# Kernel optimization log

Measured on AMD Instinct MI355X. Metric: run time of the kernel, lower is better.

Reference implementation:

```python
import jax, jax.numpy as jnp
import numpy as np

N, OBS, ENC, ACT, K = 16384, 512, 512, 64, 8
ALPHA = 1.0


def setup_inputs() -> dict:
    key = jax.random.key(0)
    ks = jax.random.split(key, 8)
    s = 0.05  # keep activations/logits well-scaled
    return {
        "X1": jax.random.normal(ks[0], (N, OBS), jnp.float32),
        "X0": jax.random.normal(ks[1], (N, OBS), jnp.float32),
        "U": jax.random.normal(ks[2], (N, ACT), jnp.float32),
        "W_enc": jax.random.normal(ks[3], (ENC, OBS), jnp.float32) * s,
        "A_all": jax.random.normal(ks[4], (K, ENC, ENC), jnp.float32) * s,
        "B_rest": jax.random.normal(ks[5], (K - 1, ACT, ENC), jnp.float32) * s,
        "C_w": jax.random.normal(ks[6], (K, ENC), jnp.float32) * s,
        "C_b": jax.random.normal(ks[7], (K,), jnp.float32) * s,
    }


def reference(X1, X0, U, W_enc, A_all, B_rest, C_w, C_b):
    enc_dim = W_enc.shape[0]
    act_dim = U.shape[1]
    k = A_all.shape[0]
    # encoder: bias-free linear
    X1e = X1 @ W_enc.T  # [N, enc]
    X0e = X0 @ W_enc.T  # [N, enc]
    # gating: argmax of linear classifier C
    inds = jnp.argmax(X0e @ C_w.T + C_b, axis=1)  # [N]
    # expert 0 uses fixed B0 = eye(enc)[:act, :]; experts 1..k-1 learned
    B0 = jnp.eye(enc_dim, dtype=X0.dtype)[:act_dim]  # [act, enc]
    B_all = jnp.concatenate([B0[None], B_rest], axis=0)  # [k, act, enc]
    # per-expert predictions for every row (nn.Linear: x @ W.T -> einsum over input dim h)
    preds = jnp.einsum('nh,keh->kne', X0e, A_all) + jnp.einsum('na,kae->kne', U, B_all)
    # squared error per (expert, row), then select each row's routed expert
    sq = jnp.sum((X1e[None, :, :] - preds) ** 2, axis=-1)  # [k, N]
    onehot = jax.nn.one_hot(inds, k, dtype=sq.dtype)  # [N, k]
    loss = ALPHA * jnp.sum(sq * onehot.T)
    return loss / (enc_dim * X1.shape[0])
```

## Files before the change

### kernel.cpp

```cpp
#include <hip/hip_runtime.h>

#define NROWS 16384
#define OBSD 512
#define ENCD 512
#define ACTD 64
#define KEXP 8

typedef __attribute__((ext_vector_type(8))) short bf16x8;
typedef __attribute__((ext_vector_type(4))) float f32x4;
typedef __attribute__((address_space(3))) unsigned char lds_byte;
typedef __attribute__((address_space(1))) unsigned char glb_byte;

__device__ __forceinline__ unsigned short f2bf(float f) {
  unsigned int u = __float_as_uint(f);
  u = (u + 0x7FFFu + ((u >> 16) & 1u)) >> 16;
  return (unsigned short)u;
}
__device__ __forceinline__ float bf2f(unsigned short h) {
  return __uint_as_float(((unsigned int)h) << 16);
}
__device__ __forceinline__ unsigned int cvtpk(float lo, float hi) {
  unsigned int r;
  asm("v_cvt_pk_bf16_f32 %0, %1, %2" : "=v"(r) : "v"(lo), "v"(hi));
  return r;
}
__device__ __forceinline__ void gload_lds16(const unsigned short* g, unsigned short* l) {
  __builtin_amdgcn_global_load_lds((const glb_byte*)g, (lds_byte*)l, 16, 0, 0);
}

__global__ __launch_bounds__(256) void prep2_k(
    const float* __restrict__ U, const float* __restrict__ W,
    const float* __restrict__ Aall, const float* __restrict__ Brest,
    const float* __restrict__ Cw,
    unsigned short* __restrict__ Ubf, unsigned short* __restrict__ Wbf,
    unsigned short* __restrict__ Abf, unsigned short* __restrict__ BfT,
    float* __restrict__ GT, float* __restrict__ loss,
    int* __restrict__ counts, int* __restrict__ cursor) {
  const int b = blockIdx.x, tid = threadIdx.x;
  if (b < 64) {
    __shared__ float red[4][64];
    int e = b >> 3, o0 = (b & 7) * 64;
    int o = tid & 63, hg = tid >> 6;
    float s = 0.f;
#pragma unroll 8
    for (int h = hg * 128; h < hg * 128 + 128; h++)
      s += Cw[e * ENCD + h] * W[(size_t)h * OBSD + o0 + o];
    red[hg][o] = s;
    __syncthreads();
    if (tid < 64)
      GT[(o0 + tid) * KEXP + e] = red[0][tid] + red[1][tid] + red[2][tid] + red[3][tid];
    return;
  }
  if (b == 64) {
    if (tid == 0) *loss = 0.f;
    if (tid < KEXP) { counts[tid] = 0; cursor[tid] = 0; }
    return;
  }
  if (b == 65) {
    for (int j = 0; j < 16; j++) {
      int i8 = j * 256 + tid;
      int e = i8 >> 3, a0 = (i8 & 7) * 8;
      unsigned int w0 = 0, w1 = 0, w2 = 0, w3 = 0;
      if (e >= a0 && e < a0 + 8) {
        unsigned int bits = 0x3F80u << ((e & 1) * 16);
        if ((e - a0) >> 1 == 0) w0 = bits;
        else if ((e - a0) >> 1 == 1) w1 = bits;
        else if ((e - a0) >> 1 == 2) w2 = bits;
        else w3 = bits;
      }
      uint4 v = {w0, w1, w2, w3};
      *(uint4*)&BfT[(size_t)i8 * 8] = v;
    }
    return;
  }
  if (b < 122) {
    __shared__ float tile[64][65];
    int t = b - 66;
    int k = (t >> 3);
    int e0 = (t & 7) * 64;
    const float* src = Brest + (size_t)k * ACTD * ENCD + e0;
#pragma unroll
    for (int j = 0; j < 16; j++) {
      int idx = j * 256 + tid;
      int a = idx >> 6, e = idx & 63;
      tile[a][e] = src[(size_t)a * ENCD + e];
    }
    __syncthreads();
    unsigned short* dst = BfT + ((size_t)(k + 1) * ENCD + e0) * ACTD;
#pragma unroll
    for (int j = 0; j < 16; j++) {
      int idx = j * 256 + tid;
      int e = idx >> 6, a = idx & 63;
      dst[(size_t)e * ACTD + a] = f2bf(tile[a][e]);
    }
    return;
  }
  int cb = b - 122;
  const float* src;
  unsigned short* dst;
  size_t i;
  if (cb < 1024)      { src = U;    dst = Ubf; i = (size_t)cb * 256 + tid; }
  else if (cb < 1280) { src = W;    dst = Wbf; i = (size_t)(cb - 1024) * 256 + tid; }
  else                { src = Aall; dst = Abf; i = (size_t)(cb - 1280) * 256 + tid; }
  float4 v = ((const float4*)src)[i];
  uint2 r = {cvtpk(v.x, v.y), cvtpk(v.z, v.w)};
  *(uint2*)&dst[i * 4] = r;
}

__global__ __launch_bounds__(256) void routing_cvt_k(
    const float* __restrict__ X0, const float* __restrict__ X1,
    const float* __restrict__ GT, const float* __restrict__ Cb,
    unsigned short* __restrict__ X0bf, unsigned short* __restrict__ X1bf,
    int* __restrict__ inds, int* __restrict__ counts) {
  const int b = blockIdx.x, tid = threadIdx.x;
  if (b >= 512) {
    size_t i = ((size_t)(b - 512) * 256 + tid) * 8;
    const float4* s4 = (const float4*)(X1 + i);
    float4 a = s4[0], c = s4[1];
    uint4 r = {cvtpk(a.x, a.y), cvtpk(a.z, a.w), cvtpk(c.x, c.y), cvtpk(c.z, c.w)};
    *(uint4*)&X1bf[i] = r;
    return;
  }
  __shared__ int lhist[KEXP];
  if (tid < KEXP) lhist[tid] = 0;
  __syncthreads();
  const int lane = tid & 63, w = tid >> 6;
  float g[8][8];
  const float* gp = GT + lane * 8 * KEXP;
#pragma unroll
  for (int j = 0; j < 8; j++) {
    float4 lo = *(const float4*)(gp + j * KEXP);
    float4 hi = *(const float4*)(gp + j * KEXP + 4);
    g[j][0] = lo.x; g[j][1] = lo.y; g[j][2] = lo.z; g[j][3] = lo.w;
    g[j][4] = hi.x; g[j][5] = hi.y; g[j][6] = hi.z; g[j][7] = hi.w;
  }
  float cb[KEXP];
#pragma unroll
  for (int e = 0; e < KEXP; e++) cb[e] = Cb[e];

#pragma unroll 2
  for (int r = 0; r < 8; r++) {
    const int n = b * 32 + w * 8 + r;
    const float4* xr = (const float4*)(X0 + (size_t)n * OBSD + lane * 8);
    float4 x = xr[0], y = xr[1];
    float xv[8] = {x.x, x.y, x.z, x.w, y.x, y.y, y.z, y.w};
    float acc[KEXP] = {};
#pragma unroll
    for (int j = 0; j < 8; j++)
#pragma unroll
      for (int e = 0; e < KEXP; e++) acc[e] += xv[j] * g[j][e];
    uint4 rr = {cvtpk(x.x, x.y), cvtpk(x.z, x.w), cvtpk(y.x, y.y), cvtpk(y.z, y.w)};
    *(uint4*)&X0bf[(size_t)n * OBSD + lane * 8] = rr;
#pragma unroll
    for (int e = 0; e < KEXP; e++) {
#pragma unroll
      for (int off = 32; off > 0; off >>= 1) acc[e] += __shfl_xor(acc[e], off, 64);
    }
    if (lane == 0) {
      int best = 0;
      float bv = acc[0] + cb[0];
#pragma unroll
      for (int e = 1; e < KEXP; e++) {
        float v = acc[e] + cb[e];
        if (v > bv) { bv = v; best = e; }
      }
      inds[n] = best;
      atomicAdd(&lhist[best], 1);
    }
  }
  __syncthreads();
  if (tid < KEXP) atomicAdd(&counts[tid], lhist[tid]);
}

__global__ void prefix_k(const int* __restrict__ counts, int* __restrict__ cursor,
                         int* __restrict__ starts) {
  if (threadIdx.x == 0 && blockIdx.x == 0) {
    int s = 0;
    for (int k = 0; k < KEXP; k++) { starts[k] = s; cursor[k] = s; s += counts[k]; }
    starts[KEXP] = s;
  }
}

__global__ __launch_bounds__(256) void scatter_k(
    const int* __restrict__ inds, int* __restrict__ cursor,
    int* __restrict__ rowlist) {
  __shared__ int lhist[KEXP], lbase[KEXP];
  const int tid = threadIdx.x;
  if (tid < KEXP) lhist[tid] = 0;
  __syncthreads();
  const int n = blockIdx.x * 256 + tid;
  const int r = inds[n];
  const int lpos = atomicAdd(&lhist[r], 1);
  __syncthreads();
  if (tid < KEXP) lbase[tid] = atomicAdd(&cursor[tid], lhist[tid]);
  __syncthreads();
  rowlist[lbase[r] + lpos] = n;
}

__global__ __launch_bounds__(256, 2) void enc_mfma_k(
    const unsigned short* __restrict__ X1bf, const unsigned short* __restrict__ X0bf,
    const unsigned short* __restrict__ Wbf, unsigned short* __restrict__ X1e,
    unsigned short* __restrict__ X0e) {
  __shared__ unsigned short As[128 * 32];
  __shared__ unsigned short Bs[128 * 32];
  const int tid = threadIdx.x;
  const int bid = blockIdx.x;
  const int lid = (bid & 7) * 128 + (bid >> 3);
  const int lz = lid >> 9;
  const int rem = lid & 511;
  const int col0 = (rem & 3) * 128;
  const int row0 = (rem >> 2) * 128;
  const unsigned short* X = lz ? X0bf : X1bf;
  unsigned short* E = lz ? X0e : X1e;

  const int lane = tid & 63, w = tid >> 6;
  const int wr = w >> 1, wc = w & 1;
  const int gslot = ((tid & 3) ^ ((tid >> 3) & 3)) * 8;
  const int srow = tid >> 2;
  const int ldsoff = tid * 8;
  const int rslot = ((lane >> 4) ^ (((lane & 15) >> 1) & 3)) * 8;
  const int arow = wr * 64 + (lane & 15);
  const int brow = wc * 64 + (lane & 15);

  f32x4 acc[4][4] = {};
  for (int k0 = 0; k0 < OBSD; k0 += 32) {
    gload_lds16(X + (size_t)(row0 + srow) * OBSD + k0 + gslot, &As[ldsoff]);
    gload_lds16(X + (size_t)(row0 + 64 + srow) * OBSD + k0 + gslot, &As[2048 + ldsoff]);
    gload_lds16(Wbf + (size_t)(col0 + srow) * OBSD + k0 + gslot, &Bs[ldsoff]);
    gload_lds16(Wbf + (size_t)(col0 + 64 + srow) * OBSD + k0 + gslot, &Bs[2048 + ldsoff]);
    __syncthreads();
    bf16x8 af[4], bfr[4];
#pragma unroll
    for (int m = 0; m < 4; m++) af[m] = *(const bf16x8*)&As[(arow + m * 16) * 32 + rslot];
#pragma unroll
    for (int n = 0; n < 4; n++) bfr[n] = *(const bf16x8*)&Bs[(brow + n * 16) * 32 + rslot];
#pragma unroll
    for (int m = 0; m < 4; m++)
#pragma unroll
      for (int n = 0; n < 4; n++)
        acc[m][n] = __builtin_amdgcn_mfma_f32_16x16x32_bf16(bfr[n], af[m], acc[m][n], 0, 0, 0);
    __syncthreads();
  }
#pragma unroll
  for (int m = 0; m < 4; m++) {
    int rowg = row0 + wr * 64 + m * 16 + (lane & 15);
#pragma unroll
    for (int n = 0; n < 4; n++) {
      int colg = col0 + wc * 64 + n * 16 + (lane >> 4) * 4;
      uint2 v = {cvtpk(acc[m][n][0], acc[m][n][1]), cvtpk(acc[m][n][2], acc[m][n][3])};
      *(uint2*)&E[(size_t)rowg * ENCD + colg] = v;
    }
  }
}

__global__ __launch_bounds__(256, 2) void grouped_mfma_k(
    const unsigned short* __restrict__ X0ebf, const unsigned short* __restrict__ X1ebf,
    const unsigned short* __restrict__ Ubf, const unsigned short* __restrict__ Abf,
    const unsigned short* __restrict__ BfTbf, const int* __restrict__ rowlist,
    const int* __restrict__ starts, float* __restrict__ loss) {
  const int tid = threadIdx.x;
  const int bid = blockIdx.x;
  const int lid = (bid & 7) * 512 + (bid >> 3);
  const int k = lid >> 9;
  const int rem = lid & 511;
  const int col0 = (rem & 3) * 128;
  const int tile = rem >> 2;

  const int start = starts[k];
  const int cnt = starts[k + 1] - start;
  if (tile * 128 >= cnt) return;

  __shared__ unsigned short As[128 * 32];
  __shared__ unsigned short Bs[128 * 32];
  __shared__ int ridx[128];
  __shared__ float red[4];

  if (tid < 128) {
    int p = tile * 128 + tid;
    ridx[tid] = rowlist[start + (p < cnt ? p : 0)];
  }
  __syncthreads();

  const int lane = tid & 63, w = tid >> 6;
  const int wr = w >> 1, wc = w & 1;
  const int gslot = ((tid & 3) ^ ((tid >> 3) & 3)) * 8;
  const int srow = tid >> 2;
  const int ldsoff = tid * 8;
  const int rslot = ((lane >> 4) ^ (((lane & 15) >> 1) & 3)) * 8;
  const int arow = wr * 64 + (lane & 15);
  const int brow = wc * 64 + (lane & 15);
  const int rn0 = ridx[srow];
  const int rn1 = ridx[64 + srow];

  f32x4 acc[4][4] = {};
  const unsigned short* Ak = Abf + (size_t)k * ENCD * ENCD;
  for (int k0 = 0; k0 < ENCD; k0 += 32) {
    gload_lds16(X0ebf + (size_t)rn0 * ENCD + k0 + gslot, &As[ldsoff]);
    gload_lds16(X0ebf + (size_t)rn1 * ENCD + k0 + gslot, &As[2048 + ldsoff]);
    gload_lds16(Ak + (size_t)(col0 + srow) * ENCD + k0 + gslot, &Bs[ldsoff]);
    gload_lds16(Ak + (size_t)(col0 + 64 + srow) * ENCD + k0 + gslot, &Bs[2048 + ldsoff]);
    __syncthreads();
    bf16x8 af[4], bfr[4];
#pragma unroll
    for (int m = 0; m < 4; m++) af[m] = *(const bf16x8*)&As[(arow + m * 16) * 32 + rslot];
#pragma unroll
    for (int n = 0; n < 4; n++) bfr[n] = *(const bf16x8*)&Bs[(brow + n * 16) * 32 + rslot];
#pragma unroll
    for (int m = 0; m < 4; m++)
#pragma unroll
      for (int n = 0; n < 4; n++)
        acc[m][n] = __builtin_amdgcn_mfma_f32_16x16x32_bf16(bfr[n], af[m], acc[m][n], 0, 0, 0);
    __syncthreads();
  }
  const unsigned short* BfTk = BfTbf + (size_t)k * ENCD * ACTD;
  for (int a0 = 0; a0 < ACTD; a0 += 32) {
    gload_lds16(Ubf + (size_t)rn0 * ACTD + a0 + gslot, &As[ldsoff]);
    gload_lds16(Ubf + (size_t)rn1 * ACTD + a0 + gslot, &As[2048 + ldsoff]);
    gload_lds16(BfTk + (size_t)(col0 + srow) * ACTD + a0 + gslot, &Bs[ldsoff]);
    gload_lds16(BfTk + (size_t)(col0 + 64 + srow) * ACTD + a0 + gslot, &Bs[2048 + ldsoff]);
    __syncthreads();
    bf16x8 af[4], bfr[4];
#pragma unroll
    for (int m = 0; m < 4; m++) af[m] = *(const bf16x8*)&As[(arow + m * 16) * 32 + rslot];
#pragma unroll
    for (int n = 0; n < 4; n++) bfr[n] = *(const bf16x8*)&Bs[(brow + n * 16) * 32 + rslot];
#pragma unroll
    for (int m = 0; m < 4; m++)
#pragma unroll
      for (int n = 0; n < 4; n++)
        acc[m][n] = __builtin_amdgcn_mfma_f32_16x16x32_bf16(bfr[n], af[m], acc[m][n], 0, 0, 0);
    __syncthreads();
  }
  float sq = 0.f;
#pragma unroll
  for (int m = 0; m < 4; m++) {
    int lr = wr * 64 + m * 16 + (lane & 15);
    bool valid = (tile * 128 + lr) < cnt;
    const unsigned short* xrow = X1ebf + (size_t)ridx[lr] * ENCD;
#pragma unroll
    for (int n = 0; n < 4; n++) {
      int cg = col0 + wc * 64 + n * 16 + (lane >> 4) * 4;
      if (valid) {
        ushort4 x4 = *(const ushort4*)&xrow[cg];
        float d0 = bf2f(x4.x) - acc[m][n][0];
        float d1 = bf2f(x4.y) - acc[m][n][1];
        float d2 = bf2f(x4.z) - acc[m][n][2];
        float d3 = bf2f(x4.w) - acc[m][n][3];
        sq += d0 * d0 + d1 * d1 + d2 * d2 + d3 * d3;
      }
    }
  }
#pragma unroll
  for (int off = 32; off > 0; off >>= 1) sq += __shfl_xor(sq, off, 64);
  if (lane == 0) red[w] = sq;
  __syncthreads();
  if (tid == 0) atomicAdd(loss, red[0] + red[1] + red[2] + red[3]);
}

__global__ void finalize_k(const float* __restrict__ loss, float* __restrict__ out) {
  if (threadIdx.x == 0 && blockIdx.x == 0)
    out[0] = loss[0] * (1.0f / ((float)ENCD * (float)NROWS));
}

extern "C" void kernel_launch(void* const* d_in, const int* in_sizes, int n_in,
                              void* d_out, int out_size, void* d_ws, size_t ws_size,
                              hipStream_t stream) {
  const float* X1 = (const float*)d_in[0];
  const float* X0 = (const float*)d_in[1];
  const float* U = (const float*)d_in[2];
  const float* W = (const float*)d_in[3];
  const float* Aall = (const float*)d_in[4];
  const float* Brest = (const float*)d_in[5];
  const float* Cw = (const float*)d_in[6];
  const float* Cb = (const float*)d_in[7];
  float* out = (float*)d_out;

  char* p = (char*)d_ws;
  auto alloc = [&](size_t bytes) { char* r = p; p += (bytes + 255) & ~(size_t)255; return r; };
  unsigned short* X1bf = (unsigned short*)alloc((size_t)NROWS * OBSD * 2);
  unsigned short* X0bf = (unsigned short*)alloc((size_t)NROWS * OBSD * 2);
  unsigned short* Ubf = (unsigned short*)alloc((size_t)NROWS * ACTD * 2);
  unsigned short* Wbf = (unsigned short*)alloc((size_t)ENCD * OBSD * 2);
  unsigned short* Abf = (unsigned short*)alloc((size_t)KEXP * ENCD * ENCD * 2);
  unsigned short* BfT = (unsigned short*)alloc((size_t)KEXP * ENCD * ACTD * 2);
  unsigned short* X1ebf = (unsigned short*)alloc((size_t)NROWS * ENCD * 2);
  unsigned short* X0ebf = (unsigned short*)alloc((size_t)NROWS * ENCD * 2);
  float* GT = (float*)alloc(KEXP * OBSD * 4);
  float* loss = (float*)alloc(256);
  int* inds = (int*)alloc(NROWS * 4);
  int* rowlist = (int*)alloc(NROWS * 4);
  int* counts = (int*)alloc(64);
  int* cursor = (int*)alloc(64);
  int* starts = (int*)alloc(64);

  prep2_k<<<3450, 256, 0, stream>>>(U, W, Aall, Brest, Cw, Ubf, Wbf, Abf, BfT,
                                    GT, loss, counts, cursor);
  routing_cvt_k<<<512 + 4096, 256, 0, stream>>>(X0, X1, GT, Cb, X0bf, X1bf,
                                                inds, counts);
  prefix_k<<<1, 1, 0, stream>>>(counts, cursor, starts);
  scatter_k<<<NROWS / 256, 256, 0, stream>>>(inds, cursor, rowlist);

  enc_mfma_k<<<1024, 256, 0, stream>>>(X1bf, X0bf, Wbf, X1ebf, X0ebf);
  grouped_mfma_k<<<4096, 256, 0, stream>>>(X0ebf, X1ebf, Ubf, Abf, BfT,
                                           rowlist, starts, loss);
  finalize_k<<<1, 64, 0, stream>>>(loss, out);
}
```

Before: 92.74 us.

## Regroup prep kernels, fuse scatter into encoder GEMM, deepen encoder K-tile

Splits out a small GT kernel and merges the weight, X1 and X0 routing conversions into one large fused prep launch. The row scatter now runs as extra blocks of the encoder GEMM kernel, removing a separate launch. The encoder GEMM K-step grows from 32 to 64 with a new 8-slot XOR swizzle, halving the barrier count per tile at the cost of doubled LDS. The net effect is fewer launches and fewer syncs, with a risk of lower occupancy from the larger shared buffers.

```diff
diff --git a/kernel.cpp b/kernel.cpp
--- a/kernel.cpp
+++ b/kernel.cpp
@@ -28,35 +28,120 @@
   __builtin_amdgcn_global_load_lds((const glb_byte*)g, (lds_byte*)l, 16, 0, 0);
 }
 
-__global__ __launch_bounds__(256) void prep2_k(
-    const float* __restrict__ U, const float* __restrict__ W,
-    const float* __restrict__ Aall, const float* __restrict__ Brest,
-    const float* __restrict__ Cw,
-    unsigned short* __restrict__ Ubf, unsigned short* __restrict__ Wbf,
-    unsigned short* __restrict__ Abf, unsigned short* __restrict__ BfT,
+__global__ __launch_bounds__(256) void gt_k(
+    const float* __restrict__ W, const float* __restrict__ Cw,
     float* __restrict__ GT, float* __restrict__ loss,
     int* __restrict__ counts, int* __restrict__ cursor) {
   const int b = blockIdx.x, tid = threadIdx.x;
-  if (b < 64) {
-    __shared__ float red[4][64];
-    int e = b >> 3, o0 = (b & 7) * 64;
-    int o = tid & 63, hg = tid >> 6;
-    float s = 0.f;
-#pragma unroll 8
-    for (int h = hg * 128; h < hg * 128 + 128; h++)
-      s += Cw[e * ENCD + h] * W[(size_t)h * OBSD + o0 + o];
-    red[hg][o] = s;
-    __syncthreads();
-    if (tid < 64)
-      GT[(o0 + tid) * KEXP + e] = red[0][tid] + red[1][tid] + red[2][tid] + red[3][tid];
-    return;
-  }
-  if (b == 64) {
+  if (b == 0) {
     if (tid == 0) *loss = 0.f;
     if (tid < KEXP) { counts[tid] = 0; cursor[tid] = 0; }
+  }
+  __shared__ float red[4][64];
+  int e = b >> 3, o0 = (b & 7) * 64;
+  int o = tid & 63, hg = tid >> 6;
+  float s = 0.f;
+#pragma unroll 8
+  for (int h = hg * 128; h < hg * 128 + 128; h++)
+    s += Cw[e * ENCD + h] * W[(size_t)h * OBSD + o0 + o];
+  red[hg][o] = s;
+  __syncthreads();
+  if (tid < 64)
+    GT[(o0 + tid) * KEXP + e] = red[0][tid] + red[1][tid] + red[2][tid] + red[3][tid];
+}
+
+__global__ __launch_bounds__(256) void fused_prep_k(
+    const float* __restrict__ X0, const float* __restrict__ X1,
+    const float* __restrict__ U, const float* __restrict__ W,
+    const float* __restrict__ Aall, const float* __restrict__ Brest,
+    const float* __restrict__ GT, const float* __restrict__ Cb,
+    unsigned short* __restrict__ X0bf, unsigned short* __restrict__ X1bf,
+    unsigned short* __restrict__ Ubf, unsigned short* __restrict__ Wbf,
+    unsigned short* __restrict__ Abf, unsigned short* __restrict__ BfT,
+    int* __restrict__ inds, int* __restrict__ counts) {
+  const int b = blockIdx.x, tid = threadIdx.x;
+  if (b < 512) {
+    __shared__ int lhist[KEXP];
+    if (tid < KEXP) lhist[tid] = 0;
+    __syncthreads();
+    const int lane = tid & 63, w = tid >> 6;
+    float g[8][8];
+    const float* gp = GT + lane * 8 * KEXP;
+#pragma unroll
+    for (int j = 0; j < 8; j++) {
+      float4 lo = *(const float4*)(gp + j * KEXP);
+      float4 hi = *(const float4*)(gp + j * KEXP + 4);
+      g[j][0] = lo.x; g[j][1] = lo.y; g[j][2] = lo.z; g[j][3] = lo.w;
+      g[j][4] = hi.x; g[j][5] = hi.y; g[j][6] = hi.z; g[j][7] = hi.w;
+    }
+    float cb[KEXP];
+#pragma unroll
+    for (int e = 0; e < KEXP; e++) cb[e] = Cb[e];
+#pragma unroll 2
+    for (int r = 0; r < 8; r++) {
+      const int n = b * 32 + w * 8 + r;
+      const float4* xr = (const float4*)(X0 + (size_t)n * OBSD + lane * 8);
+      float4 x = xr[0], y = xr[1];
+      float xv[8] = {x.x, x.y, x.z, x.w, y.x, y.y, y.z, y.w};
+      float acc[KEXP] = {};
+#pragma unroll
+      for (int j = 0; j < 8; j++)
+#pragma unroll
+        for (int e = 0; e < KEXP; e++) acc[e] += xv[j] * g[j][e];
+      uint4 rr = {cvtpk(x.x, x.y), cvtpk(x.z, x.w), cvtpk(y.x, y.y), cvtpk(y.z, y.w)};
+      *(uint4*)&X0bf[(size_t)n * OBSD + lane * 8] = rr;
+#pragma unroll
+      for (int e = 0; e < KEXP; e++) {
+#pragma unroll
+        for (int off = 32; off > 0; off >>= 1) acc[e] += __shfl_xor(acc[e], off, 64);
+      }
+      if (lane == 0) {
+        int best = 0;
+        float bv = acc[0] + cb[0];
+#pragma unroll
+        for (int e = 1; e < KEXP; e++) {
+          float v = acc[e] + cb[e];
+          if (v > bv) { bv = v; best = e; }
+        }
+        inds[n] = best;
+        atomicAdd(&lhist[best], 1);
+      }
+    }
+    __syncthreads();
+    if (tid < KEXP) atomicAdd(&counts[tid], lhist[tid]);
     return;
   }
-  if (b == 65) {
+  if (b < 4608) {
+    size_t i = ((size_t)(b - 512) * 256 + tid) * 8;
+    const float4* s4 = (const float4*)(X1 + i);
+    float4 a = s4[0], c = s4[1];
+    uint4 r = {cvtpk(a.x, a.y), cvtpk(a.z, a.w), cvtpk(c.x, c.y), cvtpk(c.z, c.w)};
+    *(uint4*)&X1bf[i] = r;
+    return;
+  }
+  if (b < 4664) {
+    __shared__ float tile[64][65];
+    int t = b - 4608;
+    int k = (t >> 3);
+    int e0 = (t & 7) * 64;
+    const float* src = Brest + (size_t)k * ACTD * ENCD + e0;
+#pragma unroll
+    for (int j = 0; j < 16; j++) {
+      int idx = j * 256 + tid;
+      int a = idx >> 6, e = idx & 63;
+      tile[a][e] = src[(size_t)a * ENCD + e];
+    }
+    __syncthreads();
+    unsigned short* dst = BfT + ((size_t)(k + 1) * ENCD + e0) * ACTD;
+#pragma unroll
+    for (int j = 0; j < 16; j++) {
+      int idx = j * 256 + tid;
+      int e = idx >> 6, a = idx & 63;
+      dst[(size_t)e * ACTD + a] = f2bf(tile[a][e]);
+    }
+    return;
+  }
+  if (b == 4664) {
     for (int j = 0; j < 16; j++) {
       int i8 = j * 256 + tid;
       int e = i8 >> 3, a0 = (i8 & 7) * 8;
@@ -73,103 +158,16 @@
     }
     return;
   }
-  if (b < 122) {
-    __shared__ float tile[64][65];
-    int t = b - 66;
-    int k = (t >> 3);
-    int e0 = (t & 7) * 64;
-    const float* src = Brest + (size_t)k * ACTD * ENCD + e0;
-#pragma unroll
-    for (int j = 0; j < 16; j++) {
-      int idx = j * 256 + tid;
-      int a = idx >> 6, e = idx & 63;
-      tile[a][e] = src[(size_t)a * ENCD + e];
-    }
-    __syncthreads();
-    unsigned short* dst = BfT + ((size_t)(k + 1) * ENCD + e0) * ACTD;
-#pragma unroll
-    for (int j = 0; j < 16; j++) {
-      int idx = j * 256 + tid;
-      int e = idx >> 6, a = idx & 63;
-      dst[(size_t)e * ACTD + a] = f2bf(tile[a][e]);
-    }
-    return;
-  }
-  int cb = b - 122;
+  int cb2 = b - 4665;
   const float* src;
   unsigned short* dst;
   size_t i;
-  if (cb < 1024)      { src = U;    dst = Ubf; i = (size_t)cb * 256 + tid; }
-  else if (cb < 1280) { src = W;    dst = Wbf; i = (size_t)(cb - 1024) * 256 + tid; }
-  else                { src = Aall; dst = Abf; i = (size_t)(cb - 1280) * 256 + tid; }
+  if (cb2 < 1024)      { src = U;    dst = Ubf; i = (size_t)cb2 * 256 + tid; }
+  else if (cb2 < 1280) { src = W;    dst = Wbf; i = (size_t)(cb2 - 1024) * 256 + tid; }
+  else                 { src = Aall; dst = Abf; i = (size_t)(cb2 - 1280) * 256 + tid; }
   float4 v = ((const float4*)src)[i];
   uint2 r = {cvtpk(v.x, v.y), cvtpk(v.z, v.w)};
   *(uint2*)&dst[i * 4] = r;
-}
-
-__global__ __launch_bounds__(256) void routing_cvt_k(
-    const float* __restrict__ X0, const float* __restrict__ X1,
-    const float* __restrict__ GT, const float* __restrict__ Cb,
-    unsigned short* __restrict__ X0bf, unsigned short* __restrict__ X1bf,
-    int* __restrict__ inds, int* __restrict__ counts) {
-  const int b = blockIdx.x, tid = threadIdx.x;
-  if (b >= 512) {
-    size_t i = ((size_t)(b - 512) * 256 + tid) * 8;
-    const float4* s4 = (const float4*)(X1 + i);
-    float4 a = s4[0], c = s4[1];
-    uint4 r = {cvtpk(a.x, a.y), cvtpk(a.z, a.w), cvtpk(c.x, c.y), cvtpk(c.z, c.w)};
-    *(uint4*)&X1bf[i] = r;
-    return;
-  }
-  __shared__ int lhist[KEXP];
-  if (tid < KEXP) lhist[tid] = 0;
-  __syncthreads();
-  const int lane = tid & 63, w = tid >> 6;
-  float g[8][8];
-  const float* gp = GT + lane * 8 * KEXP;
-#pragma unroll
-  for (int j = 0; j < 8; j++) {
-    float4 lo = *(const float4*)(gp + j * KEXP);
-    float4 hi = *(const float4*)(gp + j * KEXP + 4);
-    g[j][0] = lo.x; g[j][1] = lo.y; g[j][2] = lo.z; g[j][3] = lo.w;
-    g[j][4] = hi.x; g[j][5] = hi.y; g[j][6] = hi.z; g[j][7] = hi.w;
-  }
-  float cb[KEXP];
-#pragma unroll
-  for (int e = 0; e < KEXP; e++) cb[e] = Cb[e];
-
-#pragma unroll 2
-  for (int r = 0; r < 8; r++) {
-    const int n = b * 32 + w * 8 + r;
-    const float4* xr = (const float4*)(X0 + (size_t)n * OBSD + lane * 8);
-    float4 x = xr[0], y = xr[1];
-    float xv[8] = {x.x, x.y, x.z, x.w, y.x, y.y, y.z, y.w};
-    float acc[KEXP] = {};
-#pragma unroll
-    for (int j = 0; j < 8; j++)
-#pragma unroll
-      for (int e = 0; e < KEXP; e++) acc[e] += xv[j] * g[j][e];
-    uint4 rr = {cvtpk(x.x, x.y), cvtpk(x.z, x.w), cvtpk(y.x, y.y), cvtpk(y.z, y.w)};
-    *(uint4*)&X0bf[(size_t)n * OBSD + lane * 8] = rr;
-#pragma unroll
-    for (int e = 0; e < KEXP; e++) {
-#pragma unroll
-      for (int off = 32; off > 0; off >>= 1) acc[e] += __shfl_xor(acc[e], off, 64);
-    }
-    if (lane == 0) {
-      int best = 0;
-      float bv = acc[0] + cb[0];
-#pragma unroll
-      for (int e = 1; e < KEXP; e++) {
-        float v = acc[e] + cb[e];
-        if (v > bv) { bv = v; best = e; }
-      }
-      inds[n] = best;
-      atomicAdd(&lhist[best], 1);
-    }
-  }
-  __syncthreads();
-  if (tid < KEXP) atomicAdd(&counts[tid], lhist[tid]);
 }
 
 __global__ void prefix_k(const int* __restrict__ counts, int* __restrict__ cursor,
@@ -181,28 +179,27 @@
   }
 }
 
-__global__ __launch_bounds__(256) void scatter_k(
-    const int* __restrict__ inds, int* __restrict__ cursor,
-    int* __restrict__ rowlist) {
-  __shared__ int lhist[KEXP], lbase[KEXP];
-  const int tid = threadIdx.x;
-  if (tid < KEXP) lhist[tid] = 0;
-  __syncthreads();
-  const int n = blockIdx.x * 256 + tid;
-  const int r = inds[n];
-  const int lpos = atomicAdd(&lhist[r], 1);
-  __syncthreads();
-  if (tid < KEXP) lbase[tid] = atomicAdd(&cursor[tid], lhist[tid]);
-  __syncthreads();
-  rowlist[lbase[r] + lpos] = n;
-}
-
-__global__ __launch_bounds__(256, 2) void enc_mfma_k(
+__global__ __launch_bounds__(256, 2) void enc_scatter_k(
     const unsigned short* __restrict__ X1bf, const unsigned short* __restrict__ X0bf,
     const unsigned short* __restrict__ Wbf, unsigned short* __restrict__ X1e,
-    unsigned short* __restrict__ X0e) {
-  __shared__ unsigned short As[128 * 32];
-  __shared__ unsigned short Bs[128 * 32];
+    unsigned short* __restrict__ X0e, const int* __restrict__ inds,
+    int* __restrict__ cursor, int* __restrict__ rowlist) {
+  if (blockIdx.x >= 1024) {
+    __shared__ int lhist[KEXP], lbase[KEXP];
+    const int tid = threadIdx.x;
+    if (tid < KEXP) lhist[tid] = 0;
+    __syncthreads();
+    const int n = (blockIdx.x - 1024) * 256 + tid;
+    const int r = inds[n];
+    const int lpos = atomicAdd(&lhist[r], 1);
+    __syncthreads();
+    if (tid < KEXP) lbase[tid] = atomicAdd(&cursor[tid], lhist[tid]);
+    __syncthreads();
+    rowlist[lbase[r] + lpos] = n;
+    return;
+  }
+  __shared__ unsigned short As[128 * 64];
+  __shared__ unsigned short Bs[128 * 64];
   const int tid = threadIdx.x;
   const int bid = blockIdx.x;
   const int lid = (bid & 7) * 128 + (bid >> 3);
@@ -215,38 +212,46 @@
 
   const int lane = tid & 63, w = tid >> 6;
   const int wr = w >> 1, wc = w & 1;
-  const int gslot = ((tid & 3) ^ ((tid >> 3) & 3)) * 8;
-  const int srow = tid >> 2;
+  const int srow8 = tid >> 3;
+  const int lslot = ((tid & 7) ^ (srow8 & 7)) * 8;
   const int ldsoff = tid * 8;
-  const int rslot = ((lane >> 4) ^ (((lane & 15) >> 1) & 3)) * 8;
-  const int arow = wr * 64 + (lane & 15);
-  const int brow = wc * 64 + (lane & 15);
+  const int r15 = lane & 15;
+  const int qk = lane >> 4;
+  const int rsw = r15 & 7;
+  const int arow = wr * 64 + r15;
+  const int brow = wc * 64 + r15;
 
   f32x4 acc[4][4] = {};
-  for (int k0 = 0; k0 < OBSD; k0 += 32) {
-    gload_lds16(X + (size_t)(row0 + srow) * OBSD + k0 + gslot, &As[ldsoff]);
-    gload_lds16(X + (size_t)(row0 + 64 + srow) * OBSD + k0 + gslot, &As[2048 + ldsoff]);
-    gload_lds16(Wbf + (size_t)(col0 + srow) * OBSD + k0 + gslot, &Bs[ldsoff]);
-    gload_lds16(Wbf + (size_t)(col0 + 64 + srow) * OBSD + k0 + gslot, &Bs[2048 + ldsoff]);
-    __syncthreads();
-    bf16x8 af[4], bfr[4];
-#pragma unroll
-    for (int m = 0; m < 4; m++) af[m] = *(const bf16x8*)&As[(arow + m * 16) * 32 + rslot];
-#pragma unroll
-    for (int n = 0; n < 4; n++) bfr[n] = *(const bf16x8*)&Bs[(brow + n * 16) * 32 + rslot];
-#pragma unroll
-    for (int m = 0; m < 4; m++)
-#pragma unroll
-      for (int n = 0; n < 4; n++)
-        acc[m][n] = __builtin_amdgcn_mfma_f32_16x16x32_bf16(bfr[n], af[m], acc[m][n], 0, 0, 0);
+  for (int k0 = 0; k0 < OBSD; k0 += 64) {
+#pragma unroll
+    for (int j = 0; j < 4; j++) {
+      int row = j * 32 + srow8;
+      gload_lds16(X + (size_t)(row0 + row) * OBSD + k0 + lslot, &As[j * 2048 + ldsoff]);
+      gload_lds16(Wbf + (size_t)(col0 + row) * OBSD + k0 + lslot, &Bs[j * 2048 + ldsoff]);
+    }
+    __syncthreads();
+#pragma unroll
+    for (int kk = 0; kk < 2; kk++) {
+      const int ps = ((kk * 4 + qk) ^ rsw) * 8;
+      bf16x8 af[4], bfr[4];
+#pragma unroll
+      for (int m = 0; m < 4; m++) af[m] = *(const bf16x8*)&As[(arow + m * 16) * 64 + ps];
+#pragma unroll
+      for (int n = 0; n < 4; n++) bfr[n] = *(const bf16x8*)&Bs[(brow + n * 16) * 64 + ps];
+#pragma unroll
+      for (int m = 0; m < 4; m++)
+#pragma unroll
+        for (int n = 0; n < 4; n++)
+          acc[m][n] = __builtin_amdgcn_mfma_f32_16x16x32_bf16(bfr[n], af[m], acc[m][n], 0, 0, 0);
+    }
     __syncthreads();
   }
 #pragma unroll
   for (int m = 0; m < 4; m++) {
-    int rowg = row0 + wr * 64 + m * 16 + (lane & 15);
+    int rowg = row0 + wr * 64 + m * 16 + r15;
 #pragma unroll
     for (int n = 0; n < 4; n++) {
-      int colg = col0 + wc * 64 + n * 16 + (lane >> 4) * 4;
+      int colg = col0 + wc * 64 + n * 16 + qk * 4;
       uint2 v = {cvtpk(acc[m][n][0], acc[m][n][1]), cvtpk(acc[m][n][2], acc[m][n][3])};
       *(uint2*)&E[(size_t)rowg * ENCD + colg] = v;
     }
@@ -393,14 +398,13 @@
   int* cursor = (int*)alloc(64);
   int* starts = (int*)alloc(64);
 
-  prep2_k<<<3450, 256, 0, stream>>>(U, W, Aall, Brest, Cw, Ubf, Wbf, Abf, BfT,
-                                    GT, loss, counts, cursor);
-  routing_cvt_k<<<512 + 4096, 256, 0, stream>>>(X0, X1, GT, Cb, X0bf, X1bf,
-                                                inds, counts);
+  gt_k<<<64, 256, 0, stream>>>(W, Cw, GT, loss, counts, cursor);
+  fused_prep_k<<<7993, 256, 0, stream>>>(X0, X1, U, W, Aall, Brest, GT, Cb,
+                                         X0bf, X1bf, Ubf, Wbf, Abf, BfT,
+                                         inds, counts);
   prefix_k<<<1, 1, 0, stream>>>(counts, cursor, starts);
-  scatter_k<<<NROWS / 256, 256, 0, stream>>>(inds, cursor, rowlist);
-
-  enc_mfma_k<<<1024, 256, 0, stream>>>(X1bf, X0bf, Wbf, X1ebf, X0ebf);
+  enc_scatter_k<<<1088, 256, 0, stream>>>(X1bf, X0bf, Wbf, X1ebf, X0ebf,
+                                          inds, cursor, rowlist);
   grouped_mfma_k<<<4096, 256, 0, stream>>>(X0ebf, X1ebf, Ubf, Abf, BfT,
                                            rowlist, starts, loss);
   finalize_k<<<1, 64, 0, stream>>>(loss, out);
```

Result: faster. 87.80 us (-5.3%).
